# Kernel tuning notes

Hardware: AMD Instinct MI355X
Metric: run time of the kernel (lower is better)

Reference implementation:

```python
import jax, jax.numpy as jnp
import numpy as np

B, N, D = 16, 4096, 512   # batch, channels, d_model
R, K = 64, 128            # regions, channels per region


def setup_inputs() -> dict:
    key = jax.random.key(0)
    k1, k2, k3 = jax.random.split(key, 3)
    x = jax.random.normal(k1, (B, N, D), dtype=jnp.float32)
    region_indices = jax.random.randint(k2, (R, K), 0, N)
    W = jax.random.normal(k3, (1, D), dtype=jnp.float32) * (1.0 / np.sqrt(D))
    b = jnp.zeros((1,), dtype=jnp.float32)
    return {"x": x, "region_indices": region_indices, "W": W, "b": b}


def reference(x, region_indices, W, b):
    # Gather all regions at once: [B, R, K, D]
    xr = x[:, region_indices, :]
    # Tiny linear scorer 512 -> 1: [B, R, K]
    score = jnp.einsum('brkd,d->brk', xr, W[0]) + b[0]
    # Softmax over the K channels of each region
    attn = jax.nn.softmax(score, axis=-1)
    # Attention-weighted sum over region channels: [B, R, D]
    return jnp.einsum('brk,brkd->brd', attn, xr)
```

## Files before the change

### kernel.cpp

```cpp
#include <hip/hip_runtime.h>
#include <math.h>
#include <stdint.h>

constexpr int B = 16;
constexpr int N = 4096;
constexpr int D = 512;
constexpr int R = 64;
constexpr int K = 128;

constexpr int C    = 16;
constexpr int NC   = N / C;
constexpr int ST   = 32;
constexpr int NSUB = NC / ST;
constexpr int SLOTS = 40;

constexpr size_t OFF_CNT  = 0;
constexpr size_t OFF_ENTS = 16 * 1024;
constexpr size_t OFF_LP   = 256 * 1024;
constexpr size_t OFF_PART = 1024 * 1024;

__device__ __forceinline__ float dot4(const float4 a, const float4 b) {
    return a.x * b.x + a.y * b.y + a.z * b.z + a.w * b.w;
}

__global__ __launch_bounds__(1024) void build_inv(const int* __restrict__ idx,
                                                  int* __restrict__ cnt,
                                                  int* __restrict__ ents) {
    __shared__ int s_cnt[R * C];
    const int tid = threadIdx.x;
    s_cnt[tid] = 0;
    __syncthreads();
    #pragma unroll
    for (int i = 0; i < (R * K) / 1024; ++i) {
        const int e = i * 1024 + tid;
        const int n = idx[e];
        const int key = (e >> 7) * C + (n >> 8);
        const int slot = atomicAdd(&s_cnt[key], 1);
        if (slot < SLOTS) ents[key * SLOTS + slot] = n;
    }
    __syncthreads();
    cnt[tid] = s_cnt[tid];
}

__global__ __launch_bounds__(1024, 4) void stream_accum(
    const float* __restrict__ x,
    const float* __restrict__ W,
    const int*   __restrict__ cnt,
    const int*   __restrict__ ents,
    float* __restrict__ part,
    float* __restrict__ lp)
{
    extern __shared__ float smem[];
    const int b  = blockIdx.x >> 4;
    const int ch = blockIdx.x & 15;

    const int tid  = threadIdx.x;
    const int lane = tid & 63;
    const int wave = tid >> 6;

    const float4* W4 = (const float4*)W;
    const float4 w0 = W4[lane];
    const float4 w1 = W4[lane + 64];

    int entv0, entv1, entv2, entv3;
    {
        const int reg0 = 4 * wave;
        #define LOADB(rr, dst)                                                \
            { const int key = (reg0 + rr) * C + ch;                           \
              const int cb  = min(cnt[key], SLOTS);                           \
              dst = (lane < cb) ? ents[key * SLOTS + lane] : 0x7fffffff; }
        LOADB(0, entv0) LOADB(1, entv1) LOADB(2, entv2) LOADB(3, entv3)
        #undef LOADB
    }

    const float* xb = x + ((size_t)b * N + (size_t)ch * NC) * D;

    {
        const float4* src = (const float4*)xb;
        float4 v0 = src[tid], v1 = src[tid + 1024],
               v2 = src[tid + 2048], v3 = src[tid + 3072];
        float4* dst = (float4*)smem;
        dst[tid] = v0; dst[tid + 1024] = v1;
        dst[tid + 2048] = v2; dst[tid + 3072] = v3;
    }
    __syncthreads();

    float4 acc0[4], acc1[4];
    float  lsum[4];
    #pragma unroll
    for (int rr = 0; rr < 4; ++rr) {
        acc0[rr] = make_float4(0.f, 0.f, 0.f, 0.f);
        acc1[rr] = make_float4(0.f, 0.f, 0.f, 0.f);
        lsum[rr] = 0.f;
    }

    for (int t = 0; t < NSUB; ++t) {
        const int cur = t & 1;
        float4* buf = (float4*)(smem + cur * ST * D);
        float*  se  = smem + 2 * ST * D + cur * ST;

        {
            const int lr0 = 2 * wave, lr1 = 2 * wave + 1;
            const float4 u0 = buf[lr0 * 128 + lane], u1 = buf[lr0 * 128 + 64 + lane];
            const float4 v0 = buf[lr1 * 128 + lane], v1 = buf[lr1 * 128 + 64 + lane];
            float p = dot4(u0, w0) + dot4(u1, w1);
            float q = dot4(v0, w0) + dot4(v1, w1);
            #pragma unroll
            for (int off = 1; off < 64; off <<= 1) {
                p += __shfl_xor(p, off, 64);
                q += __shfl_xor(q, off, 64);
            }
            if (lane == 0) { se[lr0] = __expf(p); se[lr1] = __expf(q); }
        }

        float4 r0, r1, r2, r3;
        const bool have = (t + 1 < NSUB);
        if (have) {
            const float4* src = (const float4*)(xb + (size_t)(t + 1) * ST * D);
            r0 = src[tid];        r1 = src[tid + 1024];
            r2 = src[tid + 2048]; r3 = src[tid + 3072];
        }

        __syncthreads();

        const int t0 = ch * NC + t * ST;
        #define ACCUM(rr, entv)                                               \
        {                                                                     \
            unsigned long long hits =                                         \
                __ballot(entv >= t0 && entv < t0 + ST);                       \
            while (hits) {                                                    \
                const int j = (int)__builtin_ctzll(hits); hits &= hits - 1;   \
                const int lr = __shfl(entv, j, 64) - t0;                      \
                const float e = se[lr];                                       \
                const float4 u0 = buf[lr * 128 + lane];                       \
                const float4 u1 = buf[lr * 128 + 64 + lane];                  \
                acc0[rr].x += e * u0.x; acc0[rr].y += e * u0.y;               \
                acc0[rr].z += e * u0.z; acc0[rr].w += e * u0.w;               \
                acc1[rr].x += e * u1.x; acc1[rr].y += e * u1.y;               \
                acc1[rr].z += e * u1.z; acc1[rr].w += e * u1.w;               \
                lsum[rr] += e;                                                \
            }                                                                 \
        }
        ACCUM(0, entv0) ACCUM(1, entv1) ACCUM(2, entv2) ACCUM(3, entv3)
        #undef ACCUM

        if (have) {
            float4* nb = (float4*)(smem + (1 - cur) * ST * D);
            nb[tid] = r0; nb[tid + 1024] = r1;
            nb[tid + 2048] = r2; nb[tid + 3072] = r3;
        }
        __syncthreads();
    }

    #pragma unroll
    for (int rr = 0; rr < 4; ++rr) {
        const int region = 4 * wave + rr;
        float* pb = part + ((size_t)(b * R + region) * C + ch) * D;
        ((float4*)pb)[lane]      = acc0[rr];
        ((float4*)pb)[lane + 64] = acc1[rr];
        if (lane == 0) lp[(b * R + region) * C + ch] = lsum[rr];
    }
}

__global__ __launch_bounds__(512, 8) void combine(
    const float* __restrict__ part,
    const float* __restrict__ lp,
    float* __restrict__ out)
{
    const int br = blockIdx.x;
    const int d  = threadIdx.x;

    float lsum = 0.f;
    #pragma unroll
    for (int c = 0; c < C; ++c) lsum += lp[br * C + c];

    float sum = 0.f;
    #pragma unroll
    for (int c = 0; c < C; ++c)
        sum += part[((size_t)br * C + c) * D + d];

    out[(size_t)br * D + d] = sum / lsum;
}

extern "C" void kernel_launch(void* const* d_in, const int* in_sizes, int n_in,
                              void* d_out, int out_size, void* d_ws, size_t ws_size,
                              hipStream_t stream) {
    const float* x   = (const float*)d_in[0];
    const int*   idx = (const int*)d_in[1];
    const float* W   = (const float*)d_in[2];
    float* out = (float*)d_out;

    char* ws = (char*)d_ws;
    int*   cnt  = (int*)  (ws + OFF_CNT);
    int*   ents = (int*)  (ws + OFF_ENTS);
    float* lp   = (float*)(ws + OFF_LP);
    float* part = (float*)(ws + OFF_PART);

    constexpr int LDS_BYTES = (2 * ST * D + 2 * ST) * 4;
    static bool attr_set = false;
    if (!attr_set) {
        hipFuncSetAttribute(reinterpret_cast<const void*>(stream_accum),
                            hipFuncAttributeMaxDynamicSharedMemorySize, LDS_BYTES);
        attr_set = true;
    }

    build_inv   <<<1,    1024, 0,         stream>>>(idx, cnt, ents);
    stream_accum<<<B*C,  1024, LDS_BYTES, stream>>>(x, W, cnt, ents, part, lp);
    combine     <<<B*R,  512,  0,         stream>>>(part, lp, out);
}
```

Measured before the change: 210.6 us.

## Fuse inverted-index build into streaming kernel and compute scores per hit row

Drops the separate single-block build_inv kernel. Each streaming block now builds, in shared memory, only its own chunk's region-to-channel list, which removes one launch and the global cnt/ents round trip. The per-subtile score pass that wrote exp scores to shared memory is replaced by computing the dot product and exp inline for each hit row, which removes one barrier per iteration. In exchange, rows shared by several regions have their score recomputed, and each hit now does its own wave reduction. SLOTS also shrinks to 32, adding a small overflow risk for dense regions.

```diff
diff --git a/kernel.cpp b/kernel.cpp
--- a/kernel.cpp
+++ b/kernel.cpp
@@ -1,6 +1,5 @@
 #include <hip/hip_runtime.h>
 #include <math.h>
-#include <stdint.h>
 
 constexpr int B = 16;
 constexpr int N = 4096;
@@ -8,49 +7,30 @@
 constexpr int R = 64;
 constexpr int K = 128;
 
-constexpr int C    = 16;
-constexpr int NC   = N / C;
-constexpr int ST   = 32;
-constexpr int NSUB = NC / ST;
-constexpr int SLOTS = 40;
+constexpr int C     = 16;
+constexpr int NC    = N / C;
+constexpr int ST    = 32;
+constexpr int NSUB  = NC / ST;
+constexpr int SLOTS = 32;
 
-constexpr size_t OFF_CNT  = 0;
-constexpr size_t OFF_ENTS = 16 * 1024;
-constexpr size_t OFF_LP   = 256 * 1024;
+constexpr size_t OFF_LP   = 0;
 constexpr size_t OFF_PART = 1024 * 1024;
 
 __device__ __forceinline__ float dot4(const float4 a, const float4 b) {
     return a.x * b.x + a.y * b.y + a.z * b.z + a.w * b.w;
 }
 
-__global__ __launch_bounds__(1024) void build_inv(const int* __restrict__ idx,
-                                                  int* __restrict__ cnt,
-                                                  int* __restrict__ ents) {
-    __shared__ int s_cnt[R * C];
-    const int tid = threadIdx.x;
-    s_cnt[tid] = 0;
-    __syncthreads();
-    #pragma unroll
-    for (int i = 0; i < (R * K) / 1024; ++i) {
-        const int e = i * 1024 + tid;
-        const int n = idx[e];
-        const int key = (e >> 7) * C + (n >> 8);
-        const int slot = atomicAdd(&s_cnt[key], 1);
-        if (slot < SLOTS) ents[key * SLOTS + slot] = n;
-    }
-    __syncthreads();
-    cnt[tid] = s_cnt[tid];
-}
-
 __global__ __launch_bounds__(1024, 4) void stream_accum(
     const float* __restrict__ x,
+    const int*   __restrict__ idx,
     const float* __restrict__ W,
-    const int*   __restrict__ cnt,
-    const int*   __restrict__ ents,
     float* __restrict__ part,
     float* __restrict__ lp)
 {
     extern __shared__ float smem[];
+    __shared__ int s_cnt[R];
+    __shared__ int s_ents[R][SLOTS];
+
     const int b  = blockIdx.x >> 4;
     const int ch = blockIdx.x & 15;
 
@@ -62,28 +42,40 @@
     const float4 w0 = W4[lane];
     const float4 w1 = W4[lane + 64];
 
-    int entv0, entv1, entv2, entv3;
-    {
-        const int reg0 = 4 * wave;
-        #define LOADB(rr, dst)                                                \
-            { const int key = (reg0 + rr) * C + ch;                           \
-              const int cb  = min(cnt[key], SLOTS);                           \
-              dst = (lane < cb) ? ents[key * SLOTS + lane] : 0x7fffffff; }
-        LOADB(0, entv0) LOADB(1, entv1) LOADB(2, entv2) LOADB(3, entv3)
-        #undef LOADB
+    const float* xb = x + ((size_t)b * N + (size_t)ch * NC) * D;
+
+    const float4* src0 = (const float4*)xb;
+    float4 r0 = src0[tid],        r1 = src0[tid + 1024],
+           r2 = src0[tid + 2048], r3 = src0[tid + 3072];
+
+    if (tid < R) s_cnt[tid] = 0;
+    __syncthreads();
+
+    #pragma unroll
+    for (int i = 0; i < (R * K) / 1024; ++i) {
+        const int e = i * 1024 + tid;
+        const int n = idx[e];
+        if ((n >> 8) == ch) {
+            const int r = e >> 7;
+            const int s = atomicAdd(&s_cnt[r], 1);
+            if (s < SLOTS) s_ents[r][s] = n & (NC - 1);
+        }
     }
 
-    const float* xb = x + ((size_t)b * N + (size_t)ch * NC) * D;
-
     {
-        const float4* src = (const float4*)xb;
-        float4 v0 = src[tid], v1 = src[tid + 1024],
-               v2 = src[tid + 2048], v3 = src[tid + 3072];
-        float4* dst = (float4*)smem;
-        dst[tid] = v0; dst[tid + 1024] = v1;
-        dst[tid + 2048] = v2; dst[tid + 3072] = v3;
+        float4* buf0 = (float4*)smem;
+        buf0[tid] = r0; buf0[tid + 1024] = r1;
+        buf0[tid + 2048] = r2; buf0[tid + 3072] = r3;
     }
     __syncthreads();
+
+    int entv[4];
+    #pragma unroll
+    for (int rr = 0; rr < 4; ++rr) {
+        const int r  = 4 * wave + rr;
+        const int cb = min(s_cnt[r], SLOTS);
+        entv[rr] = (lane < cb) ? s_ents[r][lane] : 0x7fffffff;
+    }
 
     float4 acc0[4], acc1[4];
     float  lsum[4];
@@ -95,61 +87,44 @@
     }
 
     for (int t = 0; t < NSUB; ++t) {
-        const int cur = t & 1;
-        float4* buf = (float4*)(smem + cur * ST * D);
-        float*  se  = smem + 2 * ST * D + cur * ST;
+        float4* buf = (float4*)(smem + (t & 1) * ST * D);
+        const bool have = (t + 1 < NSUB);
 
-        {
-            const int lr0 = 2 * wave, lr1 = 2 * wave + 1;
-            const float4 u0 = buf[lr0 * 128 + lane], u1 = buf[lr0 * 128 + 64 + lane];
-            const float4 v0 = buf[lr1 * 128 + lane], v1 = buf[lr1 * 128 + 64 + lane];
-            float p = dot4(u0, w0) + dot4(u1, w1);
-            float q = dot4(v0, w0) + dot4(v1, w1);
-            #pragma unroll
-            for (int off = 1; off < 64; off <<= 1) {
-                p += __shfl_xor(p, off, 64);
-                q += __shfl_xor(q, off, 64);
-            }
-            if (lane == 0) { se[lr0] = __expf(p); se[lr1] = __expf(q); }
-        }
-
-        float4 r0, r1, r2, r3;
-        const bool have = (t + 1 < NSUB);
         if (have) {
             const float4* src = (const float4*)(xb + (size_t)(t + 1) * ST * D);
             r0 = src[tid];        r1 = src[tid + 1024];
             r2 = src[tid + 2048]; r3 = src[tid + 3072];
         }
 
-        __syncthreads();
-
-        const int t0 = ch * NC + t * ST;
-        #define ACCUM(rr, entv)                                               \
-        {                                                                     \
-            unsigned long long hits =                                         \
-                __ballot(entv >= t0 && entv < t0 + ST);                       \
-            while (hits) {                                                    \
-                const int j = (int)__builtin_ctzll(hits); hits &= hits - 1;   \
-                const int lr = __shfl(entv, j, 64) - t0;                      \
-                const float e = se[lr];                                       \
-                const float4 u0 = buf[lr * 128 + lane];                       \
-                const float4 u1 = buf[lr * 128 + 64 + lane];                  \
-                acc0[rr].x += e * u0.x; acc0[rr].y += e * u0.y;               \
-                acc0[rr].z += e * u0.z; acc0[rr].w += e * u0.w;               \
-                acc1[rr].x += e * u1.x; acc1[rr].y += e * u1.y;               \
-                acc1[rr].z += e * u1.z; acc1[rr].w += e * u1.w;               \
-                lsum[rr] += e;                                                \
-            }                                                                 \
+        const int t0 = t * ST;
+        #pragma unroll
+        for (int rr = 0; rr < 4; ++rr) {
+            unsigned long long hits =
+                __ballot(entv[rr] >= t0 && entv[rr] < t0 + ST);
+            while (hits) {
+                const int j  = (int)__builtin_ctzll(hits); hits &= hits - 1;
+                const int lr = __shfl(entv[rr], j, 64) - t0;
+                const float4 u0 = buf[lr * 128 + lane];
+                const float4 u1 = buf[lr * 128 + 64 + lane];
+                float p = dot4(u0, w0) + dot4(u1, w1);
+                #pragma unroll
+                for (int off = 1; off < 64; off <<= 1)
+                    p += __shfl_xor(p, off, 64);
+                const float e = __expf(p);
+                acc0[rr].x += e * u0.x; acc0[rr].y += e * u0.y;
+                acc0[rr].z += e * u0.z; acc0[rr].w += e * u0.w;
+                acc1[rr].x += e * u1.x; acc1[rr].y += e * u1.y;
+                acc1[rr].z += e * u1.z; acc1[rr].w += e * u1.w;
+                lsum[rr] += e;
+            }
         }
-        ACCUM(0, entv0) ACCUM(1, entv1) ACCUM(2, entv2) ACCUM(3, entv3)
-        #undef ACCUM
 
         if (have) {
-            float4* nb = (float4*)(smem + (1 - cur) * ST * D);
+            float4* nb = (float4*)(smem + ((t + 1) & 1) * ST * D);
             nb[tid] = r0; nb[tid + 1024] = r1;
             nb[tid + 2048] = r2; nb[tid + 3072] = r3;
+            __syncthreads();
         }
-        __syncthreads();
     }
 
     #pragma unroll
@@ -191,12 +166,10 @@
     float* out = (float*)d_out;
 
     char* ws = (char*)d_ws;
-    int*   cnt  = (int*)  (ws + OFF_CNT);
-    int*   ents = (int*)  (ws + OFF_ENTS);
     float* lp   = (float*)(ws + OFF_LP);
     float* part = (float*)(ws + OFF_PART);
 
-    constexpr int LDS_BYTES = (2 * ST * D + 2 * ST) * 4;
+    constexpr int LDS_BYTES = 2 * ST * D * 4;
     static bool attr_set = false;
     if (!attr_set) {
         hipFuncSetAttribute(reinterpret_cast<const void*>(stream_accum),
@@ -204,7 +177,6 @@
         attr_set = true;
     }
 
-    build_inv   <<<1,    1024, 0,         stream>>>(idx, cnt, ents);
-    stream_accum<<<B*C,  1024, LDS_BYTES, stream>>>(x, W, cnt, ents, part, lp);
-    combine     <<<B*R,  512,  0,         stream>>>(part, lp, out);
+    stream_accum<<<B * C, 1024, LDS_BYTES, stream>>>(x, idx, W, part, lp);
+    combine     <<<B * R, 512,  0,         stream>>>(part, lp, out);
 }
```

Measured after the change: 206.9 us. No clear change (-1.7%).
